# Kernel optimization log

Hardware: AMD Instinct MI355X
Metric: run time of the kernel (lower is better)

## Reference

```python
import jax, jax.numpy as jnp
import numpy as np

WINDOW = 8
HEADS = 8

def _rel_index(w):
    coords = np.stack(np.meshgrid(np.arange(w), np.arange(w), indexing='ij')).reshape(2, -1)
    rel = coords[:, :, None] - coords[:, None, :]          # [2, N, N]
    rel = rel.transpose(1, 2, 0) + (w - 1)                 # [N, N, 2]
    return jnp.asarray(rel[:, :, 0] * (2 * w - 1) + rel[:, :, 1])  # [N, N] int

def setup_inputs() -> dict:
    key = jax.random.key(0)
    ks = jax.random.split(key, 5)
    B, N, C = 4096, WINDOW * WINDOW, 256
    x = jax.random.normal(ks[0], (B, N, C), dtype=jnp.float32)
    w_qkv = jax.random.normal(ks[1], (3 * C, C), dtype=jnp.float32) * 0.02
    b_qkv = jnp.zeros((3 * C,), dtype=jnp.float32)
    bias_table = jax.random.normal(ks[2], ((2 * WINDOW - 1) ** 2, HEADS), dtype=jnp.float32) * 0.02
    w_proj = jax.random.normal(ks[3], (C, C), dtype=jnp.float32) * 0.02
    b_proj = jnp.zeros((C,), dtype=jnp.float32)
    return {"x": x, "w_qkv": w_qkv, "b_qkv": b_qkv, "bias_table": bias_table,
            "w_proj": w_proj, "b_proj": b_proj}

def reference(x, w_qkv, b_qkv, bias_table, w_proj, b_proj):
    B, N, C = x.shape
    H = HEADS
    d = C // H
    scale = d ** (-0.5)
    idx = _rel_index(WINDOW)                                # [N, N]
    qkv = x @ w_qkv.T + b_qkv                               # [B, N, 3C]
    qkv = qkv.reshape(B, N, 3, H, d).transpose(2, 0, 3, 1, 4)
    q, k, v = qkv[0], qkv[1], qkv[2]                        # [B, H, N, d]
    attn = jnp.einsum('bhnd,bhmd->bhnm', q * scale, k)      # [B, H, N, N]
    bias = bias_table[idx]                                  # [N, N, H]
    attn = attn + bias.transpose(2, 0, 1)[None]             # add per-head bias
    attn = jax.nn.softmax(attn, axis=-1)
    out = jnp.einsum('bhnm,bhmd->bhnd', attn, v)            # [B, H, N, d]
    out = out.transpose(0, 2, 1, 3).reshape(B, N, C)
    return out @ w_proj.T + b_proj
```

## Files before the change

### kernel.cpp

```cpp
#include <hip/hip_runtime.h>

typedef unsigned int u32;
typedef unsigned short u16;
typedef __bf16 bf16x8 __attribute__((ext_vector_type(8)));
typedef float f32x4 __attribute__((ext_vector_type(4)));
typedef u32 u32x4 __attribute__((ext_vector_type(4)));
typedef u32 u32x2 __attribute__((ext_vector_type(2)));

#define NTOK 64
#define CDIM 256
#define NH 8

#define WS_HDR 8
#define BIAS_O (WS_HDR)
#define WQKV_O (BIAS_O + 32768)
#define BQKV_O (WQKV_O + 196608)
#define WPRJ_O (BQKV_O + 768)
#define BPRJ_O (WPRJ_O + 65536)

#define XS_OFF 0
#define QS_OFF 33792
#define KS_OFF 67584
#define VT_OFF 101376
#define LDS_BYTES 138240

__device__ __forceinline__ float bf2f(u16 u) {
  union { u32 i; float f; } z; z.i = ((u32)u) << 16; return z.f;
}
__device__ __forceinline__ u16 f2bf(float f) {
  __bf16 h = (__bf16)f; return __builtin_bit_cast(u16, h);
}
__device__ __forceinline__ float fetchf(const void* p, int idx, int isbf) {
  return isbf ? bf2f(((const u16*)p)[idx]) : ((const float*)p)[idx];
}

__global__ void detect_dtype(const u16* __restrict__ x, int* __restrict__ flag) {
  __shared__ int cnt;
  if (threadIdx.x == 0) cnt = 0;
  __syncthreads();
  int sane = 0;
  for (int i = threadIdx.x; i < 2048; i += 256) {
    u16 u = x[2 * i];
    int e = (u >> 7) & 0xFF;
    sane += (e == 0 || (e >= 90 && e <= 160)) ? 1 : 0;
  }
  atomicAdd(&cnt, sane);
  __syncthreads();
  if (threadIdx.x == 0) *flag = (cnt >= 1638) ? 1 : 0;
}

__global__ void cvt_params(const void* __restrict__ wqkv, const void* __restrict__ bqkv,
                           const void* __restrict__ btab, const void* __restrict__ wprj,
                           const void* __restrict__ bprj, void* __restrict__ wsraw) {
  u16* ws = (u16*)wsraw;
  const int isbf = *(const int*)wsraw;
  int i = blockIdx.x * 256 + threadIdx.x;
  if (i < 32768) {
    int h = i >> 12, n = (i >> 6) & 63, m = i & 63;
    int r0 = (n >> 3) - (m >> 3) + 7, r1 = (n & 7) - (m & 7) + 7;
    ws[BIAS_O + i] = f2bf(fetchf(btab, (r0 * 15 + r1) * NH + h, isbf));
  } else if (i < 32768 + 196608) {
    int j = i - 32768;
    ws[WQKV_O + j] = f2bf(fetchf(wqkv, j, isbf));
  } else if (i < 32768 + 196608 + 768) {
    int j = i - (32768 + 196608);
    ws[BQKV_O + j] = f2bf(fetchf(bqkv, j, isbf));
  } else if (i < 32768 + 196608 + 768 + 65536) {
    int j = i - (32768 + 196608 + 768);
    ws[WPRJ_O + j] = f2bf(fetchf(wprj, j, isbf));
  } else if (i < 32768 + 196608 + 768 + 65536 + 256) {
    int j = i - (32768 + 196608 + 768 + 65536);
    ws[BPRJ_O + j] = f2bf(fetchf(bprj, j, isbf));
  }
}

__global__ __launch_bounds__(512, 2)
void win_attn_fused(const void* __restrict__ xraw, const void* __restrict__ wsraw,
                    float* __restrict__ out)
{
  __shared__ __align__(16) unsigned char lds[LDS_BYTES];
  const u16* ws  = (const u16*)wsraw;
  const int isbf = *(const int*)wsraw;
  const int b    = blockIdx.x;
  const int tid  = threadIdx.x;
  const int w    = tid >> 6;
  const int lane = tid & 63;
  const int c    = lane & 15;
  const int g    = lane >> 4;

  if (isbf) {
    const u32x4* gx = (const u32x4*)((const u16*)xraw + (size_t)b * (NTOK * CDIM));
#pragma unroll
    for (int i = 0; i < 4; ++i) {
      int q = tid + i * 512;
      int row = q >> 5, c8 = q & 31;
      *(u32x4*)(lds + XS_OFF + row * 528 + c8 * 16) = gx[q];
    }
  } else {
    const f32x4* gx = (const f32x4*)((const float*)xraw + (size_t)b * (NTOK * CDIM));
#pragma unroll
    for (int i = 0; i < 8; ++i) {
      int q = tid + i * 512;
      int row = q >> 6, c4 = q & 63;
      f32x4 v = gx[q];
      u32x2 pk;
      pk[0] = (u32)f2bf(v[0]) | ((u32)f2bf(v[1]) << 16);
      pk[1] = (u32)f2bf(v[2]) | ((u32)f2bf(v[3]) << 16);
      *(u32x2*)(lds + XS_OFF + row * 528 + c4 * 8) = pk;
    }
  }
  __syncthreads();

  const float scale = 0.1767766952966369f;

  for (int jt = 0; jt < 6; ++jt) {
    const int jc   = w * 96 + jt * 16;
    const int colw = jc + c;
    f32x4 acc[4] = {{0,0,0,0},{0,0,0,0},{0,0,0,0},{0,0,0,0}};
    const u16* wrow = ws + WQKV_O + colw * CDIM;
#pragma unroll
    for (int ks = 0; ks < 8; ++ks) {
      bf16x8 bf = *(const bf16x8*)(wrow + ks * 32 + g * 8);
#pragma unroll
      for (int rt = 0; rt < 4; ++rt) {
        bf16x8 af = *(const bf16x8*)(lds + XS_OFF + (16 * rt + c) * 528 + ks * 64 + g * 16);
        acc[rt] = __builtin_amdgcn_mfma_f32_16x16x32_bf16(af, bf, acc[rt], 0, 0, 0);
      }
    }
    const float badd = bf2f(ws[BQKV_O + colw]);
#pragma unroll
    for (int rt = 0; rt < 4; ++rt) {
#pragma unroll
      for (int reg = 0; reg < 4; ++reg) {
        int r = 16 * rt + 4 * g + reg;
        float val = acc[rt][reg] + badd;
        if (jc < 256) {
          *(u16*)(lds + QS_OFF + r * 528 + colw * 2) = f2bf(val * scale);
        } else if (jc < 512) {
          *(u16*)(lds + KS_OFF + r * 528 + (colw - 256) * 2) = f2bf(val);
        } else {
          int cc = colw - 512, hd = cc >> 5, dd = cc & 31;
          *(u16*)(lds + VT_OFF + hd * 4608 + dd * 144 + r * 2) = f2bf(val);
        }
      }
    }
  }
  __syncthreads();

  const int h = w;
  f32x4 s[4][4];
#pragma unroll
  for (int rt = 0; rt < 4; ++rt)
#pragma unroll
    for (int ct = 0; ct < 4; ++ct)
#pragma unroll
      for (int reg = 0; reg < 4; ++reg) {
        int n = 16 * rt + 4 * g + reg, m = 16 * ct + c;
        s[rt][ct][reg] = bf2f(ws[BIAS_O + (h << 12) + (n << 6) + m]);
      }
  {
    bf16x8 aq[4], bk[4];
#pragma unroll
    for (int rt = 0; rt < 4; ++rt)
      aq[rt] = *(const bf16x8*)(lds + QS_OFF + (16 * rt + c) * 528 + h * 64 + g * 16);
#pragma unroll
    for (int ct = 0; ct < 4; ++ct)
      bk[ct] = *(const bf16x8*)(lds + KS_OFF + (16 * ct + c) * 528 + h * 64 + g * 16);
#pragma unroll
    for (int rt = 0; rt < 4; ++rt)
#pragma unroll
      for (int ct = 0; ct < 4; ++ct)
        s[rt][ct] = __builtin_amdgcn_mfma_f32_16x16x32_bf16(aq[rt], bk[ct], s[rt][ct], 0, 0, 0);
  }

#pragma unroll
  for (int rt = 0; rt < 4; ++rt) {
#pragma unroll
    for (int reg = 0; reg < 4; ++reg) {
      float v0 = s[rt][0][reg], v1 = s[rt][1][reg], v2 = s[rt][2][reg], v3 = s[rt][3][reg];
      float mx = fmaxf(fmaxf(v0, v1), fmaxf(v2, v3));
#pragma unroll
      for (int i = 1; i < 16; i <<= 1) mx = fmaxf(mx, __shfl_xor(mx, i));
      v0 = __expf(v0 - mx); v1 = __expf(v1 - mx);
      v2 = __expf(v2 - mx); v3 = __expf(v3 - mx);
      float sm = v0 + v1 + v2 + v3;
#pragma unroll
      for (int i = 1; i < 16; i <<= 1) sm += __shfl_xor(sm, i);
      float inv = 1.0f / sm;
      s[rt][0][reg] = v0 * inv; s[rt][1][reg] = v1 * inv;
      s[rt][2][reg] = v2 * inv; s[rt][3][reg] = v3 * inv;
    }
  }
  __syncthreads();

  const int Pb = w * 8192;
#pragma unroll
  for (int rt = 0; rt < 4; ++rt)
#pragma unroll
    for (int ct = 0; ct < 4; ++ct)
#pragma unroll
      for (int reg = 0; reg < 4; ++reg) {
        int r = 16 * rt + 4 * g + reg, cc = 16 * ct + c;
        int byte = (r * 128 + cc * 2) ^ ((r & 7) << 4);
        *(u16*)(lds + Pb + byte) = f2bf(s[rt][ct][reg]);
      }
  __syncthreads();

  f32x4 o[4][2] = {{{0,0,0,0},{0,0,0,0}},{{0,0,0,0},{0,0,0,0}},
                   {{0,0,0,0},{0,0,0,0}},{{0,0,0,0},{0,0,0,0}}};
#pragma unroll
  for (int ks = 0; ks < 2; ++ks) {
    bf16x8 ap[4], bv[2];
#pragma unroll
    for (int rt = 0; rt < 4; ++rt) {
      int r = 16 * rt + c;
      int byte = (r * 128 + ks * 64 + g * 16) ^ ((r & 7) << 4);
      ap[rt] = *(const bf16x8*)(lds + Pb + byte);
    }
#pragma unroll
    for (int ct = 0; ct < 2; ++ct)
      bv[ct] = *(const bf16x8*)(lds + VT_OFF + h * 4608 + (16 * ct + c) * 144 + ks * 64 + g * 16);
#pragma unroll
    for (int rt = 0; rt < 4; ++rt)
#pragma unroll
      for (int ct = 0; ct < 2; ++ct)
        o[rt][ct] = __builtin_amdgcn_mfma_f32_16x16x32_bf16(ap[rt], bv[ct], o[rt][ct], 0, 0, 0);
  }
#pragma unroll
  for (int rt = 0; rt < 4; ++rt)
#pragma unroll
    for (int ct = 0; ct < 2; ++ct)
#pragma unroll
      for (int reg = 0; reg < 4; ++reg) {
        int n = 16 * rt + 4 * g + reg;
        int col = h * 32 + 16 * ct + c;
        *(u16*)(lds + KS_OFF + n * 528 + col * 2) = f2bf(o[rt][ct][reg]);
      }
  __syncthreads();

#pragma unroll
  for (int ct = 0; ct < 2; ++ct) {
    const int colw = w * 32 + ct * 16 + c;
    const float badd = bf2f(ws[BPRJ_O + colw]);
    f32x4 acc[4];
#pragma unroll
    for (int rt = 0; rt < 4; ++rt)
#pragma unroll
      for (int reg = 0; reg < 4; ++reg) acc[rt][reg] = badd;
    const u16* wrow = ws + WPRJ_O + colw * CDIM;
#pragma unroll
    for (int ks = 0; ks < 8; ++ks) {
      bf16x8 bf = *(const bf16x8*)(wrow + ks * 32 + g * 8);
#pragma unroll
      for (int rt = 0; rt < 4; ++rt) {
        bf16x8 af = *(const bf16x8*)(lds + KS_OFF + (16 * rt + c) * 528 + ks * 64 + g * 16);
        acc[rt] = __builtin_amdgcn_mfma_f32_16x16x32_bf16(af, bf, acc[rt], 0, 0, 0);
      }
    }
#pragma unroll
    for (int rt = 0; rt < 4; ++rt)
#pragma unroll
      for (int reg = 0; reg < 4; ++reg) {
        int n = 16 * rt + 4 * g + reg;
        int byte = (n * 1024 + colw * 4) ^ (((n >> 2) & 3) << 6);
        *(float*)(lds + byte) = acc[rt][reg];
      }
  }
  __syncthreads();

  float* gout = out + (size_t)b * (NTOK * CDIM);
#pragma unroll
  for (int i = 0; i < 8; ++i) {
    int q = tid + i * 512;
    int row = q >> 6, c16 = q & 63;
    f32x4 v = *(const f32x4*)(lds + ((row * 1024 + c16 * 16) ^ (((row >> 2) & 3) << 6)));
    *(f32x4*)(gout + row * CDIM + c16 * 4) = v;
  }
}

extern "C" void kernel_launch(void* const* d_in, const int* in_sizes, int n_in,
                              void* d_out, int out_size, void* d_ws, size_t ws_size,
                              hipStream_t stream) {
  (void)in_sizes; (void)n_in; (void)out_size; (void)ws_size;
  detect_dtype<<<dim3(1), dim3(256), 0, stream>>>((const u16*)d_in[0], (int*)d_ws);
  cvt_params<<<dim3(1156), dim3(256), 0, stream>>>(d_in[1], d_in[2], d_in[3], d_in[4],
                                                   d_in[5], d_ws);
  win_attn_fused<<<dim3(4096), dim3(512), 0, stream>>>(d_in[0], d_ws, (float*)d_out);
}
```

Before: 522.3 us.

## Hoist GEMM A-fragments into registers, repad LDS rows, transpose bias, drop block barrier

```diff
diff --git a/kernel.cpp b/kernel.cpp
--- a/kernel.cpp
+++ b/kernel.cpp
@@ -18,11 +18,12 @@
 #define WPRJ_O (BQKV_O + 768)
 #define BPRJ_O (WPRJ_O + 65536)
 
+#define XROW 520
 #define XS_OFF 0
-#define QS_OFF 33792
-#define KS_OFF 67584
-#define VT_OFF 101376
-#define LDS_BYTES 138240
+#define QS_OFF 33280
+#define KS_OFF 66560
+#define VT_OFF 99840
+#define LDS_BYTES 134656
 
 __device__ __forceinline__ float bf2f(u16 u) {
   union { u32 i; float f; } z; z.i = ((u32)u) << 16; return z.f;
@@ -58,7 +59,7 @@
   if (i < 32768) {
     int h = i >> 12, n = (i >> 6) & 63, m = i & 63;
     int r0 = (n >> 3) - (m >> 3) + 7, r1 = (n & 7) - (m & 7) + 7;
-    ws[BIAS_O + i] = f2bf(fetchf(btab, (r0 * 15 + r1) * NH + h, isbf));
+    ws[BIAS_O + (h << 12) + (m << 6) + n] = f2bf(fetchf(btab, (r0 * 15 + r1) * NH + h, isbf));
   } else if (i < 32768 + 196608) {
     int j = i - 32768;
     ws[WQKV_O + j] = f2bf(fetchf(wqkv, j, isbf));
@@ -94,7 +95,7 @@
     for (int i = 0; i < 4; ++i) {
       int q = tid + i * 512;
       int row = q >> 5, c8 = q & 31;
-      *(u32x4*)(lds + XS_OFF + row * 528 + c8 * 16) = gx[q];
+      *(u32x4*)(lds + XS_OFF + row * XROW + c8 * 16) = gx[q];
     }
   } else {
     const f32x4* gx = (const f32x4*)((const float*)xraw + (size_t)b * (NTOK * CDIM));
@@ -106,41 +107,48 @@
       u32x2 pk;
       pk[0] = (u32)f2bf(v[0]) | ((u32)f2bf(v[1]) << 16);
       pk[1] = (u32)f2bf(v[2]) | ((u32)f2bf(v[3]) << 16);
-      *(u32x2*)(lds + XS_OFF + row * 528 + c4 * 8) = pk;
+      *(u32x2*)(lds + XS_OFF + row * XROW + c4 * 8) = pk;
     }
   }
   __syncthreads();
 
   const float scale = 0.1767766952966369f;
 
-  for (int jt = 0; jt < 6; ++jt) {
-    const int jc   = w * 96 + jt * 16;
-    const int colw = jc + c;
-    f32x4 acc[4] = {{0,0,0,0},{0,0,0,0},{0,0,0,0},{0,0,0,0}};
-    const u16* wrow = ws + WQKV_O + colw * CDIM;
-#pragma unroll
-    for (int ks = 0; ks < 8; ++ks) {
-      bf16x8 bf = *(const bf16x8*)(wrow + ks * 32 + g * 8);
+  {
+    bf16x8 af[4][8];
+#pragma unroll
+    for (int rt = 0; rt < 4; ++rt)
+#pragma unroll
+      for (int ks = 0; ks < 8; ++ks)
+        af[rt][ks] = *(const bf16x8*)(lds + XS_OFF + (16 * rt + c) * XROW + ks * 64 + g * 16);
+
+    for (int jt = 0; jt < 6; ++jt) {
+      const int jc   = w * 96 + jt * 16;
+      const int colw = jc + c;
+      f32x4 acc[4] = {{0,0,0,0},{0,0,0,0},{0,0,0,0},{0,0,0,0}};
+      const u16* wrow = ws + WQKV_O + colw * CDIM;
+#pragma unroll
+      for (int ks = 0; ks < 8; ++ks) {
+        bf16x8 bf = *(const bf16x8*)(wrow + ks * 32 + g * 8);
+#pragma unroll
+        for (int rt = 0; rt < 4; ++rt)
+          acc[rt] = __builtin_amdgcn_mfma_f32_16x16x32_bf16(af[rt][ks], bf, acc[rt], 0, 0, 0);
+      }
+      const float badd = bf2f(ws[BQKV_O + colw]);
 #pragma unroll
       for (int rt = 0; rt < 4; ++rt) {
-        bf16x8 af = *(const bf16x8*)(lds + XS_OFF + (16 * rt + c) * 528 + ks * 64 + g * 16);
-        acc[rt] = __builtin_amdgcn_mfma_f32_16x16x32_bf16(af, bf, acc[rt], 0, 0, 0);
-      }
-    }
-    const float badd = bf2f(ws[BQKV_O + colw]);
-#pragma unroll
-    for (int rt = 0; rt < 4; ++rt) {
-#pragma unroll
-      for (int reg = 0; reg < 4; ++reg) {
-        int r = 16 * rt + 4 * g + reg;
-        float val = acc[rt][reg] + badd;
-        if (jc < 256) {
-          *(u16*)(lds + QS_OFF + r * 528 + colw * 2) = f2bf(val * scale);
-        } else if (jc < 512) {
-          *(u16*)(lds + KS_OFF + r * 528 + (colw - 256) * 2) = f2bf(val);
-        } else {
-          int cc = colw - 512, hd = cc >> 5, dd = cc & 31;
-          *(u16*)(lds + VT_OFF + hd * 4608 + dd * 144 + r * 2) = f2bf(val);
+#pragma unroll
+        for (int reg = 0; reg < 4; ++reg) {
+          int r = 16 * rt + 4 * g + reg;
+          float val = acc[rt][reg] + badd;
+          if (jc < 256) {
+            *(u16*)(lds + QS_OFF + r * XROW + colw * 2) = f2bf(val * scale);
+          } else if (jc < 512) {
+            *(u16*)(lds + KS_OFF + r * XROW + (colw - 256) * 2) = f2bf(val);
+          } else {
+            int cc = colw - 512, hd = cc >> 5, dd = cc & 31;
+            *(u16*)(lds + VT_OFF + hd * 4352 + dd * 136 + r * 2) = f2bf(val);
+          }
         }
       }
     }
@@ -152,20 +160,21 @@
 #pragma unroll
   for (int rt = 0; rt < 4; ++rt)
 #pragma unroll
-    for (int ct = 0; ct < 4; ++ct)
-#pragma unroll
-      for (int reg = 0; reg < 4; ++reg) {
-        int n = 16 * rt + 4 * g + reg, m = 16 * ct + c;
-        s[rt][ct][reg] = bf2f(ws[BIAS_O + (h << 12) + (n << 6) + m]);
-      }
+    for (int ct = 0; ct < 4; ++ct) {
+      u32x2 bp = *(const u32x2*)(ws + BIAS_O + (h << 12) + ((16 * ct + c) << 6) + 16 * rt + 4 * g);
+      s[rt][ct][0] = bf2f((u16)(bp[0] & 0xffff));
+      s[rt][ct][1] = bf2f((u16)(bp[0] >> 16));
+      s[rt][ct][2] = bf2f((u16)(bp[1] & 0xffff));
+      s[rt][ct][3] = bf2f((u16)(bp[1] >> 16));
+    }
   {
     bf16x8 aq[4], bk[4];
 #pragma unroll
     for (int rt = 0; rt < 4; ++rt)
-      aq[rt] = *(const bf16x8*)(lds + QS_OFF + (16 * rt + c) * 528 + h * 64 + g * 16);
+      aq[rt] = *(const bf16x8*)(lds + QS_OFF + (16 * rt + c) * XROW + h * 64 + g * 16);
 #pragma unroll
     for (int ct = 0; ct < 4; ++ct)
-      bk[ct] = *(const bf16x8*)(lds + KS_OFF + (16 * ct + c) * 528 + h * 64 + g * 16);
+      bk[ct] = *(const bf16x8*)(lds + KS_OFF + (16 * ct + c) * XROW + h * 64 + g * 16);
 #pragma unroll
     for (int rt = 0; rt < 4; ++rt)
 #pragma unroll
@@ -204,7 +213,7 @@
         int byte = (r * 128 + cc * 2) ^ ((r & 7) << 4);
         *(u16*)(lds + Pb + byte) = f2bf(s[rt][ct][reg]);
       }
-  __syncthreads();
+  asm volatile("" ::: "memory");
 
   f32x4 o[4][2] = {{{0,0,0,0},{0,0,0,0}},{{0,0,0,0},{0,0,0,0}},
                    {{0,0,0,0},{0,0,0,0}},{{0,0,0,0},{0,0,0,0}}};
@@ -219,7 +228,7 @@
     }
 #pragma unroll
     for (int ct = 0; ct < 2; ++ct)
-      bv[ct] = *(const bf16x8*)(lds + VT_OFF + h * 4608 + (16 * ct + c) * 144 + ks * 64 + g * 16);
+      bv[ct] = *(const bf16x8*)(lds + VT_OFF + h * 4352 + (16 * ct + c) * 136 + ks * 64 + g * 16);
 #pragma unroll
     for (int rt = 0; rt < 4; ++rt)
 #pragma unroll
@@ -234,37 +243,44 @@
       for (int reg = 0; reg < 4; ++reg) {
         int n = 16 * rt + 4 * g + reg;
         int col = h * 32 + 16 * ct + c;
-        *(u16*)(lds + KS_OFF + n * 528 + col * 2) = f2bf(o[rt][ct][reg]);
-      }
-  __syncthreads();
-
-#pragma unroll
-  for (int ct = 0; ct < 2; ++ct) {
-    const int colw = w * 32 + ct * 16 + c;
-    const float badd = bf2f(ws[BPRJ_O + colw]);
-    f32x4 acc[4];
-#pragma unroll
-    for (int rt = 0; rt < 4; ++rt)
-#pragma unroll
-      for (int reg = 0; reg < 4; ++reg) acc[rt][reg] = badd;
-    const u16* wrow = ws + WPRJ_O + colw * CDIM;
-#pragma unroll
-    for (int ks = 0; ks < 8; ++ks) {
-      bf16x8 bf = *(const bf16x8*)(wrow + ks * 32 + g * 8);
-#pragma unroll
-      for (int rt = 0; rt < 4; ++rt) {
-        bf16x8 af = *(const bf16x8*)(lds + KS_OFF + (16 * rt + c) * 528 + ks * 64 + g * 16);
-        acc[rt] = __builtin_amdgcn_mfma_f32_16x16x32_bf16(af, bf, acc[rt], 0, 0, 0);
-      }
-    }
-#pragma unroll
-    for (int rt = 0; rt < 4; ++rt)
-#pragma unroll
-      for (int reg = 0; reg < 4; ++reg) {
-        int n = 16 * rt + 4 * g + reg;
-        int byte = (n * 1024 + colw * 4) ^ (((n >> 2) & 3) << 6);
-        *(float*)(lds + byte) = acc[rt][reg];
-      }
+        *(u16*)(lds + KS_OFF + n * XROW + col * 2) = f2bf(o[rt][ct][reg]);
+      }
+  __syncthreads();
+
+  {
+    bf16x8 ay[4][8];
+#pragma unroll
+    for (int rt = 0; rt < 4; ++rt)
+#pragma unroll
+      for (int ks = 0; ks < 8; ++ks)
+        ay[rt][ks] = *(const bf16x8*)(lds + KS_OFF + (16 * rt + c) * XROW + ks * 64 + g * 16);
+
+#pragma unroll
+    for (int ct = 0; ct < 2; ++ct) {
+      const int colw = w * 32 + ct * 16 + c;
+      const float badd = bf2f(ws[BPRJ_O + colw]);
+      f32x4 acc[4];
+#pragma unroll
+      for (int rt = 0; rt < 4; ++rt)
+#pragma unroll
+        for (int reg = 0; reg < 4; ++reg) acc[rt][reg] = badd;
+      const u16* wrow = ws + WPRJ_O + colw * CDIM;
+#pragma unroll
+      for (int ks = 0; ks < 8; ++ks) {
+        bf16x8 bf = *(const bf16x8*)(wrow + ks * 32 + g * 8);
+#pragma unroll
+        for (int rt = 0; rt < 4; ++rt)
+          acc[rt] = __builtin_amdgcn_mfma_f32_16x16x32_bf16(ay[rt][ks], bf, acc[rt], 0, 0, 0);
+      }
+#pragma unroll
+      for (int rt = 0; rt < 4; ++rt)
+#pragma unroll
+        for (int reg = 0; reg < 4; ++reg) {
+          int n = 16 * rt + 4 * g + reg;
+          int byte = (n * 1024 + colw * 4) ^ (((n >> 2) & 3) << 6);
+          *(float*)(lds + byte) = acc[rt][reg];
+        }
+    }
   }
   __syncthreads();
 
```

New measurement: 556.1 us. +6.5%, slower.

## Keep Q/K/V and P in registers via lane shuffles, shrink LDS for occupancy

Applied to the files above, without the earlier changes.

```diff
diff --git a/kernel.cpp b/kernel.cpp
--- a/kernel.cpp
+++ b/kernel.cpp
@@ -18,11 +18,8 @@
 #define WPRJ_O (BQKV_O + 768)
 #define BPRJ_O (WPRJ_O + 65536)
 
-#define XS_OFF 0
-#define QS_OFF 33792
-#define KS_OFF 67584
-#define VT_OFF 101376
-#define LDS_BYTES 138240
+#define XROW 520
+#define LDS_BYTES 33280
 
 __device__ __forceinline__ float bf2f(u16 u) {
   union { u32 i; float f; } z; z.i = ((u32)u) << 16; return z.f;
@@ -30,8 +27,27 @@
 __device__ __forceinline__ u16 f2bf(float f) {
   __bf16 h = (__bf16)f; return __builtin_bit_cast(u16, h);
 }
+__device__ __forceinline__ u32 pk2(float a, float b) {
+  return (u32)f2bf(a) | ((u32)f2bf(b) << 16);
+}
 __device__ __forceinline__ float fetchf(const void* p, int idx, int isbf) {
   return isbf ? bf2f(((const u16*)p)[idx]) : ((const float*)p)[idx];
+}
+
+__device__ __forceinline__ bf16x8 frag_from(u32 p00, u32 p01, u32 p10, u32 p11,
+                                            int s0, int s1, bool hi) {
+  u32 A0 = (u32)__shfl((int)p00, s0, 64);
+  u32 A1 = (u32)__shfl((int)p01, s0, 64);
+  u32 B0 = (u32)__shfl((int)p10, s0, 64);
+  u32 B1 = (u32)__shfl((int)p11, s0, 64);
+  u32 C0 = (u32)__shfl((int)p00, s1, 64);
+  u32 C1 = (u32)__shfl((int)p01, s1, 64);
+  u32 D0 = (u32)__shfl((int)p10, s1, 64);
+  u32 D1 = (u32)__shfl((int)p11, s1, 64);
+  u32x4 f;
+  f[0] = hi ? B0 : A0;  f[1] = hi ? B1 : A1;
+  f[2] = hi ? D0 : C0;  f[3] = hi ? D1 : C1;
+  return __builtin_bit_cast(bf16x8, f);
 }
 
 __global__ void detect_dtype(const u16* __restrict__ x, int* __restrict__ flag) {
@@ -56,7 +72,7 @@
   const int isbf = *(const int*)wsraw;
   int i = blockIdx.x * 256 + threadIdx.x;
   if (i < 32768) {
-    int h = i >> 12, n = (i >> 6) & 63, m = i & 63;
+    int n = (i >> 6) & 63, m = i & 63, h = i >> 12;
     int r0 = (n >> 3) - (m >> 3) + 7, r1 = (n & 7) - (m & 7) + 7;
     ws[BIAS_O + i] = f2bf(fetchf(btab, (r0 * 15 + r1) * NH + h, isbf));
   } else if (i < 32768 + 196608) {
@@ -74,7 +90,46 @@
   }
 }
 
-__global__ __launch_bounds__(512, 2)
+#define TILE_T(PK, CHT, CHB, SCL) {                                                   \
+    bf16x8 wf[8];                                                                     \
+    const u16* wrow = ws + WQKV_O + ((CHB) + c) * CDIM;                               \
+    _Pragma("unroll")                                                                 \
+    for (int ks = 0; ks < 8; ++ks) wf[ks] = *(const bf16x8*)(wrow + ks * 32 + g * 8); \
+    f32x4 binit;                                                                      \
+    { u32x2 bp = *(const u32x2*)(ws + BQKV_O + (CHB) + 4 * g);                        \
+      binit[0] = bf2f((u16)(bp[0] & 0xffff)); binit[1] = bf2f((u16)(bp[0] >> 16));    \
+      binit[2] = bf2f((u16)(bp[1] & 0xffff)); binit[3] = bf2f((u16)(bp[1] >> 16)); }  \
+    _Pragma("unroll")                                                                 \
+    for (int nt = 0; nt < 4; ++nt) {                                                  \
+      f32x4 acc = binit;                                                              \
+      _Pragma("unroll")                                                               \
+      for (int ks = 0; ks < 8; ++ks) {                                                \
+        bf16x8 xf = *(const bf16x8*)(lds + (16 * nt + c) * XROW + ks * 64 + g * 16);  \
+        acc = __builtin_amdgcn_mfma_f32_16x16x32_bf16(wf[ks], xf, acc, 0, 0, 0);      \
+      }                                                                               \
+      PK[CHT][nt][0] = pk2(acc[0] * (SCL), acc[1] * (SCL));                           \
+      PK[CHT][nt][1] = pk2(acc[2] * (SCL), acc[3] * (SCL));                           \
+    } }
+
+#define TILE_N(PK, CHT, CHB) {                                                        \
+    bf16x8 wf[8];                                                                     \
+    const u16* wrow = ws + WQKV_O + ((CHB) + c) * CDIM;                               \
+    _Pragma("unroll")                                                                 \
+    for (int ks = 0; ks < 8; ++ks) wf[ks] = *(const bf16x8*)(wrow + ks * 32 + g * 8); \
+    const float badd = bf2f(ws[BQKV_O + (CHB) + c]);                                  \
+    _Pragma("unroll")                                                                 \
+    for (int nt = 0; nt < 4; ++nt) {                                                  \
+      f32x4 acc = {badd, badd, badd, badd};                                           \
+      _Pragma("unroll")                                                               \
+      for (int ks = 0; ks < 8; ++ks) {                                                \
+        bf16x8 xf = *(const bf16x8*)(lds + (16 * nt + c) * XROW + ks * 64 + g * 16);  \
+        acc = __builtin_amdgcn_mfma_f32_16x16x32_bf16(xf, wf[ks], acc, 0, 0, 0);      \
+      }                                                                               \
+      PK[CHT][nt][0] = pk2(acc[0], acc[1]);                                           \
+      PK[CHT][nt][1] = pk2(acc[2], acc[3]);                                           \
+    } }
+
+__global__ __launch_bounds__(512, 4)
 void win_attn_fused(const void* __restrict__ xraw, const void* __restrict__ wsraw,
                     float* __restrict__ out)
 {
@@ -87,6 +142,7 @@
   const int lane = tid & 63;
   const int c    = lane & 15;
   const int g    = lane >> 4;
+  const float scale = 0.1767766952966369f;
 
   if (isbf) {
     const u32x4* gx = (const u32x4*)((const u16*)xraw + (size_t)b * (NTOK * CDIM));
@@ -94,7 +150,7 @@
     for (int i = 0; i < 4; ++i) {
       int q = tid + i * 512;
       int row = q >> 5, c8 = q & 31;
-      *(u32x4*)(lds + XS_OFF + row * 528 + c8 * 16) = gx[q];
+      *(u32x4*)(lds + row * XROW + c8 * 16) = gx[q];
     }
   } else {
     const f32x4* gx = (const f32x4*)((const float*)xraw + (size_t)b * (NTOK * CDIM));
@@ -103,178 +159,130 @@
       int q = tid + i * 512;
       int row = q >> 6, c4 = q & 63;
       f32x4 v = gx[q];
-      u32x2 pk;
-      pk[0] = (u32)f2bf(v[0]) | ((u32)f2bf(v[1]) << 16);
-      pk[1] = (u32)f2bf(v[2]) | ((u32)f2bf(v[3]) << 16);
-      *(u32x2*)(lds + XS_OFF + row * 528 + c4 * 8) = pk;
-    }
-  }
-  __syncthreads();
-
-  const float scale = 0.1767766952966369f;
-
-  for (int jt = 0; jt < 6; ++jt) {
-    const int jc   = w * 96 + jt * 16;
-    const int colw = jc + c;
-    f32x4 acc[4] = {{0,0,0,0},{0,0,0,0},{0,0,0,0},{0,0,0,0}};
-    const u16* wrow = ws + WQKV_O + colw * CDIM;
-#pragma unroll
-    for (int ks = 0; ks < 8; ++ks) {
-      bf16x8 bf = *(const bf16x8*)(wrow + ks * 32 + g * 8);
-#pragma unroll
-      for (int rt = 0; rt < 4; ++rt) {
-        bf16x8 af = *(const bf16x8*)(lds + XS_OFF + (16 * rt + c) * 528 + ks * 64 + g * 16);
-        acc[rt] = __builtin_amdgcn_mfma_f32_16x16x32_bf16(af, bf, acc[rt], 0, 0, 0);
-      }
-    }
-    const float badd = bf2f(ws[BQKV_O + colw]);
-#pragma unroll
-    for (int rt = 0; rt < 4; ++rt) {
-#pragma unroll
-      for (int reg = 0; reg < 4; ++reg) {
-        int r = 16 * rt + 4 * g + reg;
-        float val = acc[rt][reg] + badd;
-        if (jc < 256) {
-          *(u16*)(lds + QS_OFF + r * 528 + colw * 2) = f2bf(val * scale);
-        } else if (jc < 512) {
-          *(u16*)(lds + KS_OFF + r * 528 + (colw - 256) * 2) = f2bf(val);
-        } else {
-          int cc = colw - 512, hd = cc >> 5, dd = cc & 31;
-          *(u16*)(lds + VT_OFF + hd * 4608 + dd * 144 + r * 2) = f2bf(val);
-        }
-      }
-    }
-  }
-  __syncthreads();
-
+      u32x2 pkv;
+      pkv[0] = pk2(v[0], v[1]);
+      pkv[1] = pk2(v[2], v[3]);
+      *(u32x2*)(lds + row * XROW + c4 * 8) = pkv;
+    }
+  }
+  __syncthreads();
+
+  u32 qpk[2][4][2], kpk[2][4][2], vpk[2][4][2];
+  TILE_T(qpk, 0, 32 * w,            scale);
+  TILE_T(qpk, 1, 32 * w + 16,       scale);
+  TILE_T(kpk, 0, 256 + 32 * w,      1.0f);
+  TILE_T(kpk, 1, 256 + 32 * w + 16, 1.0f);
+  TILE_N(vpk, 0, 512 + 32 * w);
+  TILE_N(vpk, 1, 512 + 32 * w + 16);
+  __syncthreads();
+
+  const int s0 = c + 32 * (g & 1), s1 = s0 + 16;
+  const bool hi = ((g >> 1) & 1) != 0;
   const int h = w;
-  f32x4 s[4][4];
-#pragma unroll
-  for (int rt = 0; rt < 4; ++rt)
-#pragma unroll
-    for (int ct = 0; ct < 4; ++ct)
-#pragma unroll
-      for (int reg = 0; reg < 4; ++reg) {
-        int n = 16 * rt + 4 * g + reg, m = 16 * ct + c;
-        s[rt][ct][reg] = bf2f(ws[BIAS_O + (h << 12) + (n << 6) + m]);
-      }
-  {
-    bf16x8 aq[4], bk[4];
-#pragma unroll
-    for (int rt = 0; rt < 4; ++rt)
-      aq[rt] = *(const bf16x8*)(lds + QS_OFF + (16 * rt + c) * 528 + h * 64 + g * 16);
-#pragma unroll
-    for (int ct = 0; ct < 4; ++ct)
-      bk[ct] = *(const bf16x8*)(lds + KS_OFF + (16 * ct + c) * 528 + h * 64 + g * 16);
-#pragma unroll
-    for (int rt = 0; rt < 4; ++rt)
-#pragma unroll
-      for (int ct = 0; ct < 4; ++ct)
-        s[rt][ct] = __builtin_amdgcn_mfma_f32_16x16x32_bf16(aq[rt], bk[ct], s[rt][ct], 0, 0, 0);
-  }
-
-#pragma unroll
-  for (int rt = 0; rt < 4; ++rt) {
-#pragma unroll
-    for (int reg = 0; reg < 4; ++reg) {
-      float v0 = s[rt][0][reg], v1 = s[rt][1][reg], v2 = s[rt][2][reg], v3 = s[rt][3][reg];
-      float mx = fmaxf(fmaxf(v0, v1), fmaxf(v2, v3));
-#pragma unroll
-      for (int i = 1; i < 16; i <<= 1) mx = fmaxf(mx, __shfl_xor(mx, i));
-      v0 = __expf(v0 - mx); v1 = __expf(v1 - mx);
-      v2 = __expf(v2 - mx); v3 = __expf(v3 - mx);
-      float sm = v0 + v1 + v2 + v3;
-#pragma unroll
-      for (int i = 1; i < 16; i <<= 1) sm += __shfl_xor(sm, i);
-      float inv = 1.0f / sm;
-      s[rt][0][reg] = v0 * inv; s[rt][1][reg] = v1 * inv;
-      s[rt][2][reg] = v2 * inv; s[rt][3][reg] = v3 * inv;
-    }
-  }
-  __syncthreads();
-
-  const int Pb = w * 8192;
-#pragma unroll
-  for (int rt = 0; rt < 4; ++rt)
-#pragma unroll
-    for (int ct = 0; ct < 4; ++ct)
-#pragma unroll
-      for (int reg = 0; reg < 4; ++reg) {
-        int r = 16 * rt + 4 * g + reg, cc = 16 * ct + c;
-        int byte = (r * 128 + cc * 2) ^ ((r & 7) << 4);
-        *(u16*)(lds + Pb + byte) = f2bf(s[rt][ct][reg]);
-      }
-  __syncthreads();
-
+
+  bf16x8 bkf[4];
+#pragma unroll
+  for (int mt = 0; mt < 4; ++mt)
+    bkf[mt] = frag_from(kpk[0][mt][0], kpk[0][mt][1], kpk[1][mt][0], kpk[1][mt][1], s0, s1, hi);
+
+  u32 Ppk[4][4][2];
+#pragma unroll
+  for (int nt = 0; nt < 4; ++nt) {
+    bf16x8 aqf = frag_from(qpk[0][nt][0], qpk[0][nt][1], qpk[1][nt][0], qpk[1][nt][1], s0, s1, hi);
+    f32x4 st[4];
+#pragma unroll
+    for (int mt = 0; mt < 4; ++mt) {
+      u32x2 bp = *(const u32x2*)(ws + BIAS_O + (h << 12) + ((16 * nt + c) << 6) + 16 * mt + 4 * g);
+      st[mt][0] = bf2f((u16)(bp[0] & 0xffff)); st[mt][1] = bf2f((u16)(bp[0] >> 16));
+      st[mt][2] = bf2f((u16)(bp[1] & 0xffff)); st[mt][3] = bf2f((u16)(bp[1] >> 16));
+    }
+#pragma unroll
+    for (int mt = 0; mt < 4; ++mt)
+      st[mt] = __builtin_amdgcn_mfma_f32_16x16x32_bf16(bkf[mt], aqf, st[mt], 0, 0, 0);
+    float mx = st[0][0];
+#pragma unroll
+    for (int mt = 0; mt < 4; ++mt)
+#pragma unroll
+      for (int r = 0; r < 4; ++r) mx = fmaxf(mx, st[mt][r]);
+    mx = fmaxf(mx, __shfl_xor(mx, 16));
+    mx = fmaxf(mx, __shfl_xor(mx, 32));
+    float sum = 0.f;
+#pragma unroll
+    for (int mt = 0; mt < 4; ++mt)
+#pragma unroll
+      for (int r = 0; r < 4; ++r) { float e = __expf(st[mt][r] - mx); st[mt][r] = e; sum += e; }
+    sum += __shfl_xor(sum, 16);
+    sum += __shfl_xor(sum, 32);
+    float inv = 1.0f / sum;
+#pragma unroll
+    for (int mt = 0; mt < 4; ++mt) {
+      Ppk[mt][nt][0] = pk2(st[mt][0] * inv, st[mt][1] * inv);
+      Ppk[mt][nt][1] = pk2(st[mt][2] * inv, st[mt][3] * inv);
+    }
+  }
+
+  bf16x8 paf[4][2];
+#pragma unroll
+  for (int nt = 0; nt < 4; ++nt)
+#pragma unroll
+    for (int k2 = 0; k2 < 2; ++k2)
+      paf[nt][k2] = frag_from(Ppk[2 * k2][nt][0], Ppk[2 * k2][nt][1],
+                              Ppk[2 * k2 + 1][nt][0], Ppk[2 * k2 + 1][nt][1], s0, s1, hi);
+  bf16x8 bvf[2][2];
+#pragma unroll
+  for (int dt = 0; dt < 2; ++dt)
+#pragma unroll
+    for (int k2 = 0; k2 < 2; ++k2)
+      bvf[dt][k2] = frag_from(vpk[dt][2 * k2][0], vpk[dt][2 * k2][1],
+                              vpk[dt][2 * k2 + 1][0], vpk[dt][2 * k2 + 1][1], s0, s1, hi);
   f32x4 o[4][2] = {{{0,0,0,0},{0,0,0,0}},{{0,0,0,0},{0,0,0,0}},
                    {{0,0,0,0},{0,0,0,0}},{{0,0,0,0},{0,0,0,0}}};
 #pragma unroll
-  for (int ks = 0; ks < 2; ++ks) {
-    bf16x8 ap[4], bv[2];
-#pragma unroll
-    for (int rt = 0; rt < 4; ++rt) {
-      int r = 16 * rt + c;
-      int byte = (r * 128 + ks * 64 + g * 16) ^ ((r & 7) << 4);
-      ap[rt] = *(const bf16x8*)(lds + Pb + byte);
-    }
-#pragma unroll
-    for (int ct = 0; ct < 2; ++ct)
-      bv[ct] = *(const bf16x8*)(lds + VT_OFF + h * 4608 + (16 * ct + c) * 144 + ks * 64 + g * 16);
-#pragma unroll
-    for (int rt = 0; rt < 4; ++rt)
-#pragma unroll
-      for (int ct = 0; ct < 2; ++ct)
-        o[rt][ct] = __builtin_amdgcn_mfma_f32_16x16x32_bf16(ap[rt], bv[ct], o[rt][ct], 0, 0, 0);
-  }
-#pragma unroll
-  for (int rt = 0; rt < 4; ++rt)
-#pragma unroll
-    for (int ct = 0; ct < 2; ++ct)
-#pragma unroll
-      for (int reg = 0; reg < 4; ++reg) {
-        int n = 16 * rt + 4 * g + reg;
-        int col = h * 32 + 16 * ct + c;
-        *(u16*)(lds + KS_OFF + n * 528 + col * 2) = f2bf(o[rt][ct][reg]);
+  for (int k2 = 0; k2 < 2; ++k2)
+#pragma unroll
+    for (int nt = 0; nt < 4; ++nt) {
+      o[nt][0] = __builtin_amdgcn_mfma_f32_16x16x32_bf16(paf[nt][k2], bvf[0][k2], o[nt][0], 0, 0, 0);
+      o[nt][1] = __builtin_amdgcn_mfma_f32_16x16x32_bf16(paf[nt][k2], bvf[1][k2], o[nt][1], 0, 0, 0);
+    }
+
+#pragma unroll
+  for (int nt = 0; nt < 4; ++nt)
+#pragma unroll
+    for (int dt = 0; dt < 2; ++dt)
+#pragma unroll
+      for (int r = 0; r < 4; ++r) {
+        int n = 16 * nt + 4 * g + r, col = 32 * w + 16 * dt + c;
+        *(u16*)(lds + n * XROW + col * 2) = f2bf(o[nt][dt][r]);
       }
   __syncthreads();
 
+  float* gout = out + (size_t)b * (NTOK * CDIM);
 #pragma unroll
   for (int ct = 0; ct < 2; ++ct) {
-    const int colw = w * 32 + ct * 16 + c;
+    const int colw = 32 * w + 16 * ct + c;
     const float badd = bf2f(ws[BPRJ_O + colw]);
     f32x4 acc[4];
 #pragma unroll
     for (int rt = 0; rt < 4; ++rt)
 #pragma unroll
-      for (int reg = 0; reg < 4; ++reg) acc[rt][reg] = badd;
+      for (int r = 0; r < 4; ++r) acc[rt][r] = badd;
     const u16* wrow = ws + WPRJ_O + colw * CDIM;
 #pragma unroll
     for (int ks = 0; ks < 8; ++ks) {
-      bf16x8 bf = *(const bf16x8*)(wrow + ks * 32 + g * 8);
+      bf16x8 wf = *(const bf16x8*)(wrow + ks * 32 + g * 8);
 #pragma unroll
       for (int rt = 0; rt < 4; ++rt) {
-        bf16x8 af = *(const bf16x8*)(lds + KS_OFF + (16 * rt + c) * 528 + ks * 64 + g * 16);
-        acc[rt] = __builtin_amdgcn_mfma_f32_16x16x32_bf16(af, bf, acc[rt], 0, 0, 0);
+        bf16x8 ay = *(const bf16x8*)(lds + (16 * rt + c) * XROW + ks * 64 + g * 16);
+        acc[rt] = __builtin_amdgcn_mfma_f32_16x16x32_bf16(ay, wf, acc[rt], 0, 0, 0);
       }
     }
 #pragma unroll
     for (int rt = 0; rt < 4; ++rt)
 #pragma unroll
-      for (int reg = 0; reg < 4; ++reg) {
-        int n = 16 * rt + 4 * g + reg;
-        int byte = (n * 1024 + colw * 4) ^ (((n >> 2) & 3) << 6);
-        *(float*)(lds + byte) = acc[rt][reg];
+      for (int r = 0; r < 4; ++r) {
+        int n = 16 * rt + 4 * g + r;
+        gout[n * CDIM + colw] = acc[rt][r];
       }
-  }
-  __syncthreads();
-
-  float* gout = out + (size_t)b * (NTOK * CDIM);
-#pragma unroll
-  for (int i = 0; i < 8; ++i) {
-    int q = tid + i * 512;
-    int row = q >> 6, c16 = q & 63;
-    f32x4 v = *(const f32x4*)(lds + ((row * 1024 + c16 * 16) ^ (((row >> 2) & 3) << 6)));
-    *(f32x4*)(gout + row * CDIM + c16 * 4) = v;
   }
 }
 
```

After: 661.6 us. +26.7%, slower.
